# Optimization experiments

Hardware: AMD Instinct MI355X
Metric: run time of the kernel (lower is better)

## Reference

```python
import jax, jax.numpy as jnp
import numpy as np
from jax import lax

START, STOP, NTAGS = 18, 19, 20
NEG = -10000.0
V, E, H, L = 100000, 300, 512, 512  # vocab, embed_dim, per-direction hidden, seq_len


def setup_inputs() -> dict:
    key = jax.random.key(0)
    ks = jax.random.split(key, 16)
    f = lambda k, s: jax.random.normal(k, s, dtype=jnp.float32) * 0.05
    trans = jax.random.normal(ks[14], (NTAGS, NTAGS), dtype=jnp.float32)
    trans = trans.at[START, :].set(NEG).at[:, STOP].set(NEG)
    return {
        "sentence": jax.random.randint(ks[0], (L,), 0, V),
        "embed_table": f(ks[1], (V, E)),
        "w_ih_f": f(ks[2], (4 * H, E)), "w_hh_f": f(ks[3], (4 * H, H)),
        "b_ih_f": f(ks[4], (4 * H,)), "b_hh_f": f(ks[5], (4 * H,)),
        "w_ih_b": f(ks[6], (4 * H, E)), "w_hh_b": f(ks[7], (4 * H, H)),
        "b_ih_b": f(ks[8], (4 * H,)), "b_hh_b": f(ks[9], (4 * H,)),
        "h0": f(ks[10], (2, H)), "c0": f(ks[11], (2, H)),
        "w_out": f(ks[12], (NTAGS, 2 * H)), "b_out": f(ks[13], (NTAGS,)),
        "transitions": trans,
    }


def _lstm_dir(x, wih, whh, bih, bhh, h0, c0, reverse):
    # x: [L, E]; PyTorch gate order i, f, g, o
    b = bih + bhh
    def step(carry, xt):
        h, c = carry
        g = xt @ wih.T + h @ whh.T + b  # [4H]
        i, fg, gg, o = jnp.split(g, 4)
        c = jax.nn.sigmoid(fg) * c + jax.nn.sigmoid(i) * jnp.tanh(gg)
        h = jax.nn.sigmoid(o) * jnp.tanh(c)
        return (h, c), h
    _, hs = lax.scan(step, (h0, c0), x, reverse=reverse)
    return hs  # [L, H] in time order


def _lstm_feats(sentence, embed_table, w_ih_f, w_hh_f, b_ih_f, b_hh_f,
                w_ih_b, w_hh_b, b_ih_b, b_hh_b, h0, c0, w_out, b_out):
    x = embed_table[sentence]  # [L, E]
    hf = _lstm_dir(x, w_ih_f, w_hh_f, b_ih_f, b_hh_f, h0[0], c0[0], False)
    hb = _lstm_dir(x, w_ih_b, w_hh_b, b_ih_b, b_hh_b, h0[1], c0[1], True)
    h = jnp.concatenate([hf, hb], axis=-1)  # [L, 2H]
    return h @ w_out.T + b_out  # [L, NTAGS]


def reference(sentence, embed_table, w_ih_f, w_hh_f, b_ih_f, b_hh_f,
              w_ih_b, w_hh_b, b_ih_b, b_hh_b, h0, c0, w_out, b_out, transitions):
    feats = _lstm_feats(sentence, embed_table, w_ih_f, w_hh_f, b_ih_f, b_hh_f,
                        w_ih_b, w_hh_b, b_ih_b, b_hh_b, h0, c0, w_out, b_out)
    init = jnp.full((NTAGS,), NEG, dtype=feats.dtype).at[START].set(0.0)

    def vstep(fv, feat):
        scores = fv[None, :] + transitions  # [next_tag, prev_tag]
        bptr = jnp.argmax(scores, axis=1)
        return jnp.max(scores, axis=1) + feat, bptr

    fv, bptrs = lax.scan(vstep, init, feats)  # bptrs: [L, NTAGS]
    terminal = fv + transitions[STOP]
    best = jnp.argmax(terminal)

    def back(tag, bp):
        # tag is the best tag at step t; bp maps tag_t -> tag_{t-1}
        return bp[tag], tag

    _, path = lax.scan(back, best, bptrs, reverse=True)  # [L] in time order
    return path
```

## Files before the change

kernel.cpp:

```cpp
#include <hip/hip_runtime.h>
#include <math.h>

#define L 512
#define E 300
#define H 512
#define G4H 2048
#define NTAGS 20
#define START_TAG 18
#define STOP_TAG 19

#define GPD 32
#define HPW 16
#define KSL 64

#define OFF_XW    0u
#define OFF_XBUF  8388608u
#define OFF_HIST  9003008u
#define OFF_FEATS 11100160u
#define OFF_HBUF  11182080u

__global__ void k0_gather(const int* __restrict__ sentence,
                          const float* __restrict__ embed,
                          float* __restrict__ xbuf) {
    int t = blockIdx.x;
    int tid = threadIdx.x;
    size_t row = (size_t)sentence[t] * E;
    for (int k = tid; k < E; k += 256)
        xbuf[(size_t)t * E + k] = embed[row + k];
}

__global__ void k1_xw(const float* __restrict__ wih_f, const float* __restrict__ wih_b,
                      const float* __restrict__ bih_f, const float* __restrict__ bhh_f,
                      const float* __restrict__ bih_b, const float* __restrict__ bhh_b,
                      const float* __restrict__ xbuf, float* __restrict__ xw) {
    __shared__ float x8[8][304];
    int tid = threadIdx.x;
    int n   = blockIdx.x * 256 + tid;
    int t0  = blockIdx.y * 8;
    int dir = blockIdx.z;
    const float* wih = dir ? wih_b : wih_f;
    const float* bih = dir ? bih_b : bih_f;
    const float* bhh = dir ? bhh_b : bhh_f;

    for (int r = 0; r < 8; ++r)
        for (int k = tid; k < E; k += 256)
            x8[r][k] = xbuf[(size_t)(t0 + r) * E + k];
    __syncthreads();

    const float* wrow = wih + (size_t)n * E;
    double acc[8];
#pragma unroll
    for (int r = 0; r < 8; ++r) acc[r] = 0.0;

    for (int k = 0; k < E; k += 4) {
        float4 wv = *(const float4*)(wrow + k);
#pragma unroll
        for (int r = 0; r < 8; ++r) {
            float4 xv = *(const float4*)(&x8[r][k]);
            acc[r] = fma((double)wv.x, (double)xv.x, acc[r]);
            acc[r] = fma((double)wv.y, (double)xv.y, acc[r]);
            acc[r] = fma((double)wv.z, (double)xv.z, acc[r]);
            acc[r] = fma((double)wv.w, (double)xv.w, acc[r]);
        }
    }
    double bias = (double)bih[n] + (double)bhh[n];
#pragma unroll
    for (int r = 0; r < 8; ++r)
        xw[((size_t)(dir * L) + (t0 + r)) * G4H + n] = (float)(acc[r] + bias);
}

__global__ __launch_bounds__(512) void k2_lstm(
    const float* __restrict__ whh_f, const float* __restrict__ whh_b,
    const float* __restrict__ h0, const float* __restrict__ c0,
    const float* __restrict__ xw, float* __restrict__ hist,
    unsigned long long* __restrict__ hbuf) {
    const int bid = blockIdx.x;
    const int dir = bid >> 5;
    const int wg  = bid & 31;
    const int tid = threadIdx.x;
    const int lr  = tid >> 3;
    const int q   = tid & 7;
    const int gt  = lr >> 4;
    const int jj  = lr & 15;
    const int gr  = gt * H + wg * HPW + jj;

    const float* whh = dir ? whh_b : whh_f;
    const float* xwd = xw + (size_t)dir * L * G4H;
    float* histd = hist + (size_t)dir * L * H;
    unsigned long long* hb = hbuf + dir * 1024;

    float w[KSL];
    {
        const float* wp = whh + (size_t)gr * H + q * KSL;
#pragma unroll
        for (int i = 0; i < KSL; i += 4) {
            float4 v = *(const float4*)(wp + i);
            w[i] = v.x; w[i + 1] = v.y; w[i + 2] = v.z; w[i + 3] = v.w;
        }
    }

    __shared__ double hs[8 * 66];
    __shared__ double gbuf[64];

    double c = 0.0;
    if (tid < HPW) c = (double)c0[dir * H + wg * HPW + tid];

    for (int s = 1; s <= L; ++s) {
        const int t = dir ? (L - s) : (s - 1);

        if (s == 1) {
            float f = h0[dir * H + tid];
            hs[(tid >> 6) * 66 + (tid & 63)] = (double)f;
        } else {
            unsigned long long* slot = hb + (((s - 1) & 1) << 9) + tid;
            unsigned long long u;
            while (((u = __hip_atomic_load(slot, __ATOMIC_RELAXED,
                                           __HIP_MEMORY_SCOPE_AGENT)) >> 32)
                   != (unsigned)(s - 1))
                __builtin_amdgcn_s_sleep(1);
            hs[(tid >> 6) * 66 + (tid & 63)] =
                (double)__uint_as_float((unsigned)(u & 0xffffffffu));
        }
        __syncthreads();

        double acc = 0.0;
        const double* hp = hs + q * 66;
#pragma unroll
        for (int i = 0; i < KSL; i += 2) {
            double2 h2 = *(const double2*)(hp + i);
            acc = fma((double)w[i],     h2.x, acc);
            acc = fma((double)w[i + 1], h2.y, acc);
        }
        acc += __shfl_xor(acc, 1, 8);
        acc += __shfl_xor(acc, 2, 8);
        acc += __shfl_xor(acc, 4, 8);
        if (q == 0) gbuf[lr] = acc;
        __syncthreads();

        if (tid < 64) {
            int gate = tid >> 4, j = tid & 15;
            double pre = gbuf[tid] +
                (double)xwd[(size_t)t * G4H + gate * H + wg * HPW + j];
            double a  = (gate == 2) ? 2.0 * pre : pre;
            double sg = 1.0 / (1.0 + exp(-a));
            double v  = (gate == 2) ? (2.0 * sg - 1.0) : sg;
            double ig = __shfl(v, j);
            double fg = __shfl(v, j + 16);
            double gg = __shfl(v, j + 32);
            double og = __shfl(v, j + 48);
            if (tid < 16) {
                c = fg * c + ig * gg;
                double s2 = 1.0 / (1.0 + exp(-2.0 * c));
                double h  = og * (2.0 * s2 - 1.0);
                float hf = (float)h;
                histd[(size_t)t * H + wg * HPW + tid] = hf;
                unsigned long long u =
                    ((unsigned long long)(unsigned)s << 32) |
                    (unsigned long long)__float_as_uint(hf);
                __hip_atomic_store(hb + ((s & 1) << 9) + wg * HPW + tid, u,
                                   __ATOMIC_RELAXED, __HIP_MEMORY_SCOPE_AGENT);
            }
        }
    }
}

__global__ void k3_feats(const float* __restrict__ hist,
                         const float* __restrict__ wout,
                         const float* __restrict__ bout,
                         double* __restrict__ feats) {
    int t = blockIdx.x;
    int tid = threadIdx.x;
    int tag = tid >> 4;
    int part = tid & 15;
    const float* h0p = hist + (size_t)t * H;
    const float* h1p = hist + (size_t)L * H + (size_t)t * H;
    int j0 = part * 64;
    double acc = 0.0;
    for (int jj = 0; jj < 64; jj += 4) {
        int j = j0 + jj;
        float4 w4 = *(const float4*)(wout + (size_t)tag * (2 * H) + j);
        float4 h4 = (j < H) ? *(const float4*)(h0p + j)
                            : *(const float4*)(h1p + (j - H));
        acc = fma((double)w4.x, (double)h4.x, acc);
        acc = fma((double)w4.y, (double)h4.y, acc);
        acc = fma((double)w4.z, (double)h4.z, acc);
        acc = fma((double)w4.w, (double)h4.w, acc);
    }
    acc += __shfl_xor(acc, 8, 16);
    acc += __shfl_xor(acc, 4, 16);
    acc += __shfl_xor(acc, 2, 16);
    acc += __shfl_xor(acc, 1, 16);
    if (part == 0) feats[(size_t)t * NTAGS + tag] = acc + (double)bout[tag];
}

__global__ void k4_viterbi(const double* __restrict__ feats,
                           const float* __restrict__ trans,
                           int* __restrict__ out) {
    __shared__ double trl[NTAGS * NTAGS];
    __shared__ double fv[2][NTAGS];
    __shared__ unsigned char bp[L][NTAGS];
    int tid = threadIdx.x;
    for (int i = tid; i < NTAGS * NTAGS; i += 64)
        trl[i] = (double)trans[i];
    if (tid < NTAGS) fv[0][tid] = (tid == START_TAG) ? 0.0 : -10000.0;
    __syncthreads();

    double nf = (tid < NTAGS) ? feats[tid] : 0.0;
    int cur = 0;
    for (int t = 0; t < L; ++t) {
        double f = nf;
        if (tid < NTAGS && t + 1 < L) nf = feats[(size_t)(t + 1) * NTAGS + tid];
        if (tid < NTAGS) {
            double best = -1.0e300;
            int b = 0;
#pragma unroll
            for (int pt = 0; pt < NTAGS; ++pt) {
                double sc = fv[cur][pt] + trl[tid * NTAGS + pt];
                if (sc > best) { best = sc; b = pt; }
            }
            fv[cur ^ 1][tid] = best + f;
            bp[t][tid] = (unsigned char)b;
        }
        __syncthreads();
        cur ^= 1;
    }
    if (tid == 0) {
        double best = -1.0e300;
        int bt = 0;
        for (int pt = 0; pt < NTAGS; ++pt) {
            double sc = fv[cur][pt] + trl[STOP_TAG * NTAGS + pt];
            if (sc > best) { best = sc; bt = pt; }
        }
        int tag = bt;
        out[L - 1] = tag;
        for (int t = L - 1; t >= 1; --t) {
            tag = bp[t][tag];
            out[t - 1] = tag;
        }
    }
}

extern "C" void kernel_launch(void* const* d_in, const int* in_sizes, int n_in,
                              void* d_out, int out_size, void* d_ws, size_t ws_size,
                              hipStream_t stream) {
    const int*   sentence = (const int*)d_in[0];
    const float* embed    = (const float*)d_in[1];
    const float* wih_f    = (const float*)d_in[2];
    const float* whh_f    = (const float*)d_in[3];
    const float* bih_f    = (const float*)d_in[4];
    const float* bhh_f    = (const float*)d_in[5];
    const float* wih_b    = (const float*)d_in[6];
    const float* whh_b    = (const float*)d_in[7];
    const float* bih_b    = (const float*)d_in[8];
    const float* bhh_b    = (const float*)d_in[9];
    const float* h0       = (const float*)d_in[10];
    const float* c0       = (const float*)d_in[11];
    const float* wout     = (const float*)d_in[12];
    const float* bout     = (const float*)d_in[13];
    const float* trans    = (const float*)d_in[14];
    int* out = (int*)d_out;

    char* ws = (char*)d_ws;
    float*  xw    = (float*)(ws + OFF_XW);
    float*  xbuf  = (float*)(ws + OFF_XBUF);
    float*  hist  = (float*)(ws + OFF_HIST);
    double* feats = (double*)(ws + OFF_FEATS);
    unsigned long long* hbuf = (unsigned long long*)(ws + OFF_HBUF);

    k0_gather<<<L, 256, 0, stream>>>(sentence, embed, xbuf);
    k1_xw<<<dim3(8, 64, 2), 256, 0, stream>>>(wih_f, wih_b, bih_f, bhh_f,
                                              bih_b, bhh_b, xbuf, xw);
    {
        void* args[] = {(void*)&whh_f, (void*)&whh_b, (void*)&h0, (void*)&c0,
                        (void*)&xw, (void*)&hist, (void*)&hbuf};
        hipLaunchCooperativeKernel((const void*)k2_lstm, dim3(2 * GPD), dim3(512),
                                   args, 0, stream);
    }
    k3_feats<<<L, 320, 0, stream>>>(hist, wout, bout, feats);
    k4_viterbi<<<1, 64, 0, stream>>>(feats, trans, out);
}
```

Baseline: 1.623 ms.

## Switch pipeline to fp32, fuse gather into input GEMM, restructure LSTM and Viterbi

Replaces double-precision accumulation with fp32 throughout the input projection, the recurrent LSTM step, the feature projection and Viterbi. The embedding gather kernel is folded into the input projection, which now reads embedding rows directly with 16 timesteps per block. The LSTM step broadcasts h through readlane instead of a shared-memory double buffer, with one partial-sum stage through LDS, and prefetches the xw row early. Viterbi now runs as a single-wavefront register/shuffle version. Dropping fp64 trades numerical headroom for speed and could change argmax ties in the decoded path.

```diff
diff --git a/kernel.cpp b/kernel.cpp
--- a/kernel.cpp
+++ b/kernel.cpp
@@ -11,62 +11,52 @@
 
 #define GPD 32
 #define HPW 16
-#define KSL 64
+#define TR  16
 
 #define OFF_XW    0u
-#define OFF_XBUF  8388608u
-#define OFF_HIST  9003008u
-#define OFF_FEATS 11100160u
-#define OFF_HBUF  11182080u
-
-__global__ void k0_gather(const int* __restrict__ sentence,
-                          const float* __restrict__ embed,
-                          float* __restrict__ xbuf) {
-    int t = blockIdx.x;
-    int tid = threadIdx.x;
-    size_t row = (size_t)sentence[t] * E;
-    for (int k = tid; k < E; k += 256)
-        xbuf[(size_t)t * E + k] = embed[row + k];
-}
-
-__global__ void k1_xw(const float* __restrict__ wih_f, const float* __restrict__ wih_b,
+#define OFF_HIST  8388608u
+#define OFF_HBUF  10485760u
+#define OFF_FEATS 10502144u
+
+__global__ void k1_xw(const int* __restrict__ sentence,
+                      const float* __restrict__ embed,
+                      const float* __restrict__ wih_f, const float* __restrict__ wih_b,
                       const float* __restrict__ bih_f, const float* __restrict__ bhh_f,
                       const float* __restrict__ bih_b, const float* __restrict__ bhh_b,
-                      const float* __restrict__ xbuf, float* __restrict__ xw) {
-    __shared__ float x8[8][304];
+                      float* __restrict__ xw) {
     int tid = threadIdx.x;
     int n   = blockIdx.x * 256 + tid;
-    int t0  = blockIdx.y * 8;
+    int t0  = blockIdx.y * TR;
     int dir = blockIdx.z;
     const float* wih = dir ? wih_b : wih_f;
     const float* bih = dir ? bih_b : bih_f;
     const float* bhh = dir ? bhh_b : bhh_f;
-
-    for (int r = 0; r < 8; ++r)
-        for (int k = tid; k < E; k += 256)
-            x8[r][k] = xbuf[(size_t)(t0 + r) * E + k];
-    __syncthreads();
-
     const float* wrow = wih + (size_t)n * E;
-    double acc[8];
-#pragma unroll
-    for (int r = 0; r < 8; ++r) acc[r] = 0.0;
-
-    for (int k = 0; k < E; k += 4) {
-        float4 wv = *(const float4*)(wrow + k);
-#pragma unroll
-        for (int r = 0; r < 8; ++r) {
-            float4 xv = *(const float4*)(&x8[r][k]);
-            acc[r] = fma((double)wv.x, (double)xv.x, acc[r]);
-            acc[r] = fma((double)wv.y, (double)xv.y, acc[r]);
-            acc[r] = fma((double)wv.z, (double)xv.z, acc[r]);
-            acc[r] = fma((double)wv.w, (double)xv.w, acc[r]);
-        }
-    }
-    double bias = (double)bih[n] + (double)bhh[n];
-#pragma unroll
-    for (int r = 0; r < 8; ++r)
-        xw[((size_t)(dir * L) + (t0 + r)) * G4H + n] = (float)(acc[r] + bias);
+
+    const float* xr[TR];
+#pragma unroll
+    for (int r = 0; r < TR; ++r)
+        xr[r] = embed + (size_t)sentence[t0 + r] * E;
+
+    float acc[TR];
+#pragma unroll
+    for (int r = 0; r < TR; ++r) acc[r] = 0.f;
+
+    for (int kk = 0; kk < E / 4; ++kk) {
+        float4 wv = ((const float4*)wrow)[kk];
+#pragma unroll
+        for (int r = 0; r < TR; ++r) {
+            float4 xv = ((const float4*)xr[r])[kk];
+            acc[r] = fmaf(wv.x, xv.x,
+                     fmaf(wv.y, xv.y,
+                     fmaf(wv.z, xv.z,
+                     fmaf(wv.w, xv.w, acc[r]))));
+        }
+    }
+    float b = bih[n] + bhh[n];
+#pragma unroll
+    for (int r = 0; r < TR; ++r)
+        xw[((size_t)(dir * L) + (t0 + r)) * G4H + n] = acc[r] + b;
 }
 
 __global__ __launch_bounds__(512) void k2_lstm(
@@ -78,39 +68,38 @@
     const int dir = bid >> 5;
     const int wg  = bid & 31;
     const int tid = threadIdx.x;
-    const int lr  = tid >> 3;
-    const int q   = tid & 7;
-    const int gt  = lr >> 4;
-    const int jj  = lr & 15;
-    const int gr  = gt * H + wg * HPW + jj;
+    const int wv  = tid >> 6;
+    const int l   = tid & 63;
+    const int gate = l >> 4;
+    const int j    = l & 15;
+    const int row  = gate * H + wg * HPW + j;
 
     const float* whh = dir ? whh_b : whh_f;
     const float* xwd = xw + (size_t)dir * L * G4H;
     float* histd = hist + (size_t)dir * L * H;
     unsigned long long* hb = hbuf + dir * 1024;
 
-    float w[KSL];
+    float w[64];
     {
-        const float* wp = whh + (size_t)gr * H + q * KSL;
-#pragma unroll
-        for (int i = 0; i < KSL; i += 4) {
+        const float* wp = whh + (size_t)row * H + wv * 64;
+#pragma unroll
+        for (int i = 0; i < 64; i += 4) {
             float4 v = *(const float4*)(wp + i);
             w[i] = v.x; w[i + 1] = v.y; w[i + 2] = v.z; w[i + 3] = v.w;
         }
     }
 
-    __shared__ double hs[8 * 66];
-    __shared__ double gbuf[64];
-
-    double c = 0.0;
-    if (tid < HPW) c = (double)c0[dir * H + wg * HPW + tid];
+    __shared__ float pbuf[2][8][64];
+
+    float c = (tid < HPW) ? c0[dir * H + wg * HPW + tid] : 0.f;
 
     for (int s = 1; s <= L; ++s) {
         const int t = dir ? (L - s) : (s - 1);
-
+        float xg = xwd[(size_t)t * G4H + row];
+
+        float hval;
         if (s == 1) {
-            float f = h0[dir * H + tid];
-            hs[(tid >> 6) * 66 + (tid & 63)] = (double)f;
+            hval = h0[dir * H + tid];
         } else {
             unsigned long long* slot = hb + (((s - 1) & 1) << 9) + tid;
             unsigned long long u;
@@ -118,45 +107,39 @@
                                            __HIP_MEMORY_SCOPE_AGENT)) >> 32)
                    != (unsigned)(s - 1))
                 __builtin_amdgcn_s_sleep(1);
-            hs[(tid >> 6) * 66 + (tid & 63)] =
-                (double)__uint_as_float((unsigned)(u & 0xffffffffu));
-        }
+            hval = __uint_as_float((unsigned)u);
+        }
+
+        float acc = 0.f;
+#pragma unroll
+        for (int i = 0; i < 64; ++i) {
+            float hb_i = __uint_as_float(
+                (unsigned)__builtin_amdgcn_readlane((int)__float_as_uint(hval), i));
+            acc = fmaf(w[i], hb_i, acc);
+        }
+        pbuf[s & 1][wv][l] = acc;
         __syncthreads();
 
-        double acc = 0.0;
-        const double* hp = hs + q * 66;
-#pragma unroll
-        for (int i = 0; i < KSL; i += 2) {
-            double2 h2 = *(const double2*)(hp + i);
-            acc = fma((double)w[i],     h2.x, acc);
-            acc = fma((double)w[i + 1], h2.y, acc);
-        }
-        acc += __shfl_xor(acc, 1, 8);
-        acc += __shfl_xor(acc, 2, 8);
-        acc += __shfl_xor(acc, 4, 8);
-        if (q == 0) gbuf[lr] = acc;
-        __syncthreads();
-
         if (tid < 64) {
-            int gate = tid >> 4, j = tid & 15;
-            double pre = gbuf[tid] +
-                (double)xwd[(size_t)t * G4H + gate * H + wg * HPW + j];
-            double a  = (gate == 2) ? 2.0 * pre : pre;
-            double sg = 1.0 / (1.0 + exp(-a));
-            double v  = (gate == 2) ? (2.0 * sg - 1.0) : sg;
-            double ig = __shfl(v, j);
-            double fg = __shfl(v, j + 16);
-            double gg = __shfl(v, j + 32);
-            double og = __shfl(v, j + 48);
-            if (tid < 16) {
+            float g = 0.f;
+#pragma unroll
+            for (int p = 0; p < 8; ++p) g += pbuf[s & 1][p][l];
+            float pre = g + xg;
+            float a  = (gate == 2) ? 2.f * pre : pre;
+            float sg = 1.f / (1.f + __expf(-a));
+            float v  = (gate == 2) ? (2.f * sg - 1.f) : sg;
+            float ig = __shfl(v, j);
+            float fg = __shfl(v, j + 16);
+            float gg = __shfl(v, j + 32);
+            float og = __shfl(v, j + 48);
+            if (tid < HPW) {
                 c = fg * c + ig * gg;
-                double s2 = 1.0 / (1.0 + exp(-2.0 * c));
-                double h  = og * (2.0 * s2 - 1.0);
-                float hf = (float)h;
-                histd[(size_t)t * H + wg * HPW + tid] = hf;
+                float tc = 2.f / (1.f + __expf(-2.f * c)) - 1.f;
+                float h  = og * tc;
+                histd[(size_t)t * H + wg * HPW + tid] = h;
                 unsigned long long u =
                     ((unsigned long long)(unsigned)s << 32) |
-                    (unsigned long long)__float_as_uint(hf);
+                    (unsigned long long)__float_as_uint(h);
                 __hip_atomic_store(hb + ((s & 1) << 9) + wg * HPW + tid, u,
                                    __ATOMIC_RELAXED, __HIP_MEMORY_SCOPE_AGENT);
             }
@@ -167,7 +150,7 @@
 __global__ void k3_feats(const float* __restrict__ hist,
                          const float* __restrict__ wout,
                          const float* __restrict__ bout,
-                         double* __restrict__ feats) {
+                         float* __restrict__ feats) {
     int t = blockIdx.x;
     int tid = threadIdx.x;
     int tag = tid >> 4;
@@ -175,66 +158,64 @@
     const float* h0p = hist + (size_t)t * H;
     const float* h1p = hist + (size_t)L * H + (size_t)t * H;
     int j0 = part * 64;
-    double acc = 0.0;
+    float acc = 0.f;
     for (int jj = 0; jj < 64; jj += 4) {
         int j = j0 + jj;
         float4 w4 = *(const float4*)(wout + (size_t)tag * (2 * H) + j);
         float4 h4 = (j < H) ? *(const float4*)(h0p + j)
                             : *(const float4*)(h1p + (j - H));
-        acc = fma((double)w4.x, (double)h4.x, acc);
-        acc = fma((double)w4.y, (double)h4.y, acc);
-        acc = fma((double)w4.z, (double)h4.z, acc);
-        acc = fma((double)w4.w, (double)h4.w, acc);
+        acc = fmaf(w4.x, h4.x, fmaf(w4.y, h4.y,
+              fmaf(w4.z, h4.z, fmaf(w4.w, h4.w, acc))));
     }
     acc += __shfl_xor(acc, 8, 16);
     acc += __shfl_xor(acc, 4, 16);
     acc += __shfl_xor(acc, 2, 16);
     acc += __shfl_xor(acc, 1, 16);
-    if (part == 0) feats[(size_t)t * NTAGS + tag] = acc + (double)bout[tag];
-}
-
-__global__ void k4_viterbi(const double* __restrict__ feats,
+    if (part == 0) feats[(size_t)t * NTAGS + tag] = acc + bout[tag];
+}
+
+__global__ void k4_viterbi(const float* __restrict__ feats,
                            const float* __restrict__ trans,
                            int* __restrict__ out) {
-    __shared__ double trl[NTAGS * NTAGS];
-    __shared__ double fv[2][NTAGS];
-    __shared__ unsigned char bp[L][NTAGS];
-    int tid = threadIdx.x;
-    for (int i = tid; i < NTAGS * NTAGS; i += 64)
-        trl[i] = (double)trans[i];
-    if (tid < NTAGS) fv[0][tid] = (tid == START_TAG) ? 0.0 : -10000.0;
-    __syncthreads();
-
-    double nf = (tid < NTAGS) ? feats[tid] : 0.0;
-    int cur = 0;
+    __shared__ unsigned char bp[L * NTAGS];
+    int lane = threadIdx.x;
+    bool act = lane < NTAGS;
+
+    float trl[NTAGS];
+#pragma unroll
+    for (int p = 0; p < NTAGS; ++p)
+        trl[p] = act ? trans[lane * NTAGS + p] : -1.0e30f;
+
+    float fv = (lane == START_TAG) ? 0.f : -10000.f;
+    float nf = act ? feats[lane] : 0.f;
+
     for (int t = 0; t < L; ++t) {
-        double f = nf;
-        if (tid < NTAGS && t + 1 < L) nf = feats[(size_t)(t + 1) * NTAGS + tid];
-        if (tid < NTAGS) {
-            double best = -1.0e300;
-            int b = 0;
-#pragma unroll
-            for (int pt = 0; pt < NTAGS; ++pt) {
-                double sc = fv[cur][pt] + trl[tid * NTAGS + pt];
-                if (sc > best) { best = sc; b = pt; }
-            }
-            fv[cur ^ 1][tid] = best + f;
-            bp[t][tid] = (unsigned char)b;
-        }
-        __syncthreads();
-        cur ^= 1;
-    }
-    if (tid == 0) {
-        double best = -1.0e300;
-        int bt = 0;
-        for (int pt = 0; pt < NTAGS; ++pt) {
-            double sc = fv[cur][pt] + trl[STOP_TAG * NTAGS + pt];
-            if (sc > best) { best = sc; bt = pt; }
-        }
-        int tag = bt;
+        float f = nf;
+        if (act && t + 1 < L) nf = feats[(size_t)(t + 1) * NTAGS + lane];
+        float best = -1.0e30f;
+        int b = 0;
+#pragma unroll
+        for (int p = 0; p < NTAGS; ++p) {
+            float sc = __shfl(fv, p) + trl[p];
+            if (sc > best) { best = sc; b = p; }
+        }
+        fv = best + f;
+        if (act) bp[t * NTAGS + lane] = (unsigned char)b;
+    }
+
+    float ts = act ? fv + trans[STOP_TAG * NTAGS + lane] : -1.0e30f;
+    int bi = lane;
+#pragma unroll
+    for (int off = 32; off; off >>= 1) {
+        float ov = __shfl_down(ts, off);
+        int   oi = __shfl_down(bi, off);
+        if (ov > ts) { ts = ov; bi = oi; }
+    }
+    if (lane == 0) {
+        int tag = bi;
         out[L - 1] = tag;
         for (int t = L - 1; t >= 1; --t) {
-            tag = bp[t][tag];
+            tag = bp[t * NTAGS + tag];
             out[t - 1] = tag;
         }
     }
@@ -261,15 +242,13 @@
     int* out = (int*)d_out;
 
     char* ws = (char*)d_ws;
-    float*  xw    = (float*)(ws + OFF_XW);
-    float*  xbuf  = (float*)(ws + OFF_XBUF);
-    float*  hist  = (float*)(ws + OFF_HIST);
-    double* feats = (double*)(ws + OFF_FEATS);
+    float* xw    = (float*)(ws + OFF_XW);
+    float* hist  = (float*)(ws + OFF_HIST);
+    float* feats = (float*)(ws + OFF_FEATS);
     unsigned long long* hbuf = (unsigned long long*)(ws + OFF_HBUF);
 
-    k0_gather<<<L, 256, 0, stream>>>(sentence, embed, xbuf);
-    k1_xw<<<dim3(8, 64, 2), 256, 0, stream>>>(wih_f, wih_b, bih_f, bhh_f,
-                                              bih_b, bhh_b, xbuf, xw);
+    k1_xw<<<dim3(8, 32, 2), 256, 0, stream>>>(sentence, embed, wih_f, wih_b,
+                                              bih_f, bhh_f, bih_b, bhh_b, xw);
     {
         void* args[] = {(void*)&whh_f, (void*)&whh_b, (void*)&h0, (void*)&c0,
                         (void*)&xw, (void*)&hist, (void*)&hbuf};
```

After: 1.498 ms. 7.7% less time.
